# Kernel tuning notes

Hardware: AMD Instinct MI355X
Metric: run time of the kernel (lower is better)

The kernel has to match this reference:

```python
import jax, jax.numpy as jnp
import numpy as np

B, WIN, NN, F_IN, H = 8, 12, 2000, 8, 64
N = B * WIN * NN          # total graph nodes = 192000
E = 2_000_000             # edges
EPS = 1e-5                # BatchNorm eps
FC1_IN = 2 * H + WIN * F_IN + 1  # 225


def setup_inputs() -> dict:
    key = jax.random.key(0)
    ks = jax.random.split(key, 24)
    s = lambda k, shp: (jax.random.normal(k, shp, jnp.float32) * 0.05)
    d = {}
    d["adj_indices"] = jax.random.randint(ks[0], (2, E), 0, N)
    d["adj_weight"] = jax.random.uniform(ks[1], (E,), jnp.float32)
    d["x"] = jax.random.normal(ks[2], (N, F_IN), jnp.float32)
    d["inner_out"] = jax.random.normal(ks[3], (B * NN,), jnp.float32)
    # GCN layers
    d["W1"] = s(ks[4], (F_IN, H)); d["b1"] = jnp.zeros((H,), jnp.float32)
    d["W2"] = s(ks[5], (H, H));    d["b2"] = jnp.zeros((H,), jnp.float32)
    # BatchNorm affine params
    d["g1"] = jnp.ones((H,), jnp.float32);  d["be1"] = jnp.zeros((H,), jnp.float32)
    d["g2"] = jnp.ones((H,), jnp.float32);  d["be2"] = jnp.zeros((H,), jnp.float32)
    # LSTM 1 (input 2H) and LSTM 2 (input H); torch gate order i,f,g,o
    d["Wih1"] = s(ks[6], (4 * H, 2 * H)); d["Whh1"] = s(ks[7], (4 * H, H))
    d["bih1"] = jnp.zeros((4 * H,), jnp.float32); d["bhh1"] = jnp.zeros((4 * H,), jnp.float32)
    d["Wih2"] = s(ks[8], (4 * H, H)); d["Whh2"] = s(ks[9], (4 * H, H))
    d["bih2"] = jnp.zeros((4 * H,), jnp.float32); d["bhh2"] = jnp.zeros((4 * H,), jnp.float32)
    # FC head
    d["fc1_w"] = s(ks[10], (FC1_IN, H)); d["fc1_b"] = jnp.zeros((H,), jnp.float32)
    d["fc3_w"] = s(ks[11], (H, 1));      d["fc3_b"] = jnp.zeros((1,), jnp.float32)
    return d


def gcn(x, W, b, row, col, w):
    # PyG GCNConv: add self loops (weight 1), symmetric deg^-1/2 normalization,
    # aggregate messages from row (source) into col (target).
    loop = jnp.arange(N)
    r = jnp.concatenate([row, loop])
    c = jnp.concatenate([col, loop])
    ww = jnp.concatenate([w, jnp.ones((N,), w.dtype)])
    deg = jax.ops.segment_sum(ww, c, num_segments=N)
    dis = jnp.where(deg > 0, 1.0 / jnp.sqrt(deg), 0.0)
    norm = dis[r] * ww * dis[c]                      # [E+N]
    h = x @ W                                        # [N,H]
    out = jax.ops.segment_sum(h[r] * norm[:, None], c, num_segments=N)
    return out + b


def bn(x, g, b):  # training-mode BatchNorm1d (batch stats, biased var)
    m = x.mean(0)
    v = x.var(0)
    return (x - m) / jnp.sqrt(v + EPS) * g + b


def lstm(xs, Wih, Whh, bih, bhh):
    # xs: [T, Bn, D]; returns (all hidden states [T,Bn,H], last hidden [Bn,H])
    Bn = xs.shape[1]
    h0 = jnp.zeros((Bn, H), xs.dtype)
    def step(carry, xt):
        h, c = carry
        gates = xt @ Wih.T + h @ Whh.T + bih + bhh
        i, f, g, o = jnp.split(gates, 4, axis=-1)
        c = jax.nn.sigmoid(f) * c + jax.nn.sigmoid(i) * jnp.tanh(g)
        h = jax.nn.sigmoid(o) * jnp.tanh(c)
        return (h, c), h
    (hT, _), ys = jax.lax.scan(step, (h0, h0), xs)
    return ys, hT


def reference(adj_indices, adj_weight, x, inner_out,
              W1, b1, W2, b2, g1, be1, g2, be2,
              Wih1, Whh1, bih1, bhh1, Wih2, Whh2, bih2, bhh2,
              fc1_w, fc1_b, fc3_w, fc3_b):
    row, col = adj_indices[0], adj_indices[1]
    skip = x.reshape(B, WIN, NN, F_IN).transpose(0, 2, 1, 3).reshape(B * NN, WIN * F_IN)
    h1 = bn(jax.nn.relu(gcn(x, W1, b1, row, col, adj_weight)), g1, be1)   # dropout = identity (eval)
    h2 = bn(jax.nn.relu(gcn(h1, W2, b2, row, col, adj_weight)), g2, be2)
    h = jnp.concatenate([h1, h2], axis=1)                                  # [N, 2H]
    seq = h.reshape(B, WIN, NN, 2 * H).transpose(1, 0, 2, 3).reshape(WIN, B * NN, 2 * H)
    y1, hn1 = lstm(seq, Wih1, Whh1, bih1, bhh1)
    _, hn2 = lstm(y1, Wih2, Whh2, bih2, bhh2)
    z = jnp.concatenate([hn1, hn2, inner_out[:, None], skip], axis=1)      # [B*NN, FC1_IN]
    z = jax.nn.relu(z @ fc1_w + fc1_b)
    z = jax.nn.relu(z @ fc3_w + fc3_b)
    return z.reshape(-1)                                                   # [B*NN]
```

## Files before the change

### kernel.cpp

```cpp
#include <hip/hip_runtime.h>
#include <math.h>

#define N_NODES 192000
#define EDGES   2000000
#define HID     64
#define BN_ROWS 16000
#define T_WIN   12
#define B_SZ    8
#define NN_SZ   2000
#define FIN     8
#define BN_EPS  1e-5f

typedef _Float16 f16x2 __attribute__((ext_vector_type(2)));
typedef _Float16 half4 __attribute__((ext_vector_type(4)));
typedef _Float16 half8 __attribute__((ext_vector_type(8)));
typedef float    f32x4 __attribute__((ext_vector_type(4)));
union F16x2U { float f; f16x2 h; };

__device__ __forceinline__ float frcp(float x){
#if __has_builtin(__builtin_amdgcn_rcpf)
    return __builtin_amdgcn_rcpf(x);
#else
    return 1.0f/x;
#endif
}
__device__ __forceinline__ float fsig(float x){ return frcp(1.0f + __expf(-x)); }
__device__ __forceinline__ float ftanh(float x){ return fmaf(2.0f, fsig(2.0f*x), -1.0f); }

__device__ __forceinline__ float packf16(float a, float b){
    F16x2U u; u.h[0] = (_Float16)a; u.h[1] = (_Float16)b; return u.f;
}

__global__ void edge_pre(const int* __restrict__ col, const float* __restrict__ w,
                         unsigned long long* __restrict__ dc, int* __restrict__ rank){
    int e = blockIdx.x*blockDim.x + threadIdx.x;
    if (e < EDGES){
        int c = col[e];
        unsigned int fx = (unsigned int)(w[e]*16777216.0f + 0.5f);
        unsigned long long old = atomicAdd(&dc[c], (1ULL << 32) | (unsigned long long)fx);
        rank[e] = (int)(old >> 32);
    }
}

__global__ void scanA(const unsigned long long* __restrict__ dc,
                      int* __restrict__ excl, int* __restrict__ bsum){
    __shared__ int sm[256];
    int i = blockIdx.x*256 + threadIdx.x;
    int v = (int)(dc[i] >> 32);
    sm[threadIdx.x] = v;
    __syncthreads();
    #pragma unroll
    for (int off = 1; off < 256; off <<= 1){
        int t = (threadIdx.x >= off) ? sm[threadIdx.x - off] : 0;
        __syncthreads();
        sm[threadIdx.x] += t;
        __syncthreads();
    }
    excl[i] = sm[threadIdx.x] - v;
    if (threadIdx.x == 255) bsum[blockIdx.x] = sm[255];
}

__global__ void scanB(const int* __restrict__ bsum, int* __restrict__ bscan, int nb){
    __shared__ int sm[1024];
    int tid = threadIdx.x;
    int v = (tid < nb) ? bsum[tid] : 0;
    sm[tid] = v;
    __syncthreads();
    #pragma unroll
    for (int off = 1; off < 1024; off <<= 1){
        int t = (tid >= off) ? sm[tid - off] : 0;
        __syncthreads();
        sm[tid] += t;
        __syncthreads();
    }
    bscan[tid] = sm[tid] - v;
}

__global__ void scanC(const int* __restrict__ excl, const int* __restrict__ bscan,
                      const unsigned long long* __restrict__ dc,
                      float* __restrict__ dis, int* __restrict__ offsets){
    int i = blockIdx.x*256 + threadIdx.x;
    offsets[i] = excl[i] + bscan[i >> 8];
    float deg = (float)(unsigned int)(dc[i] & 0xffffffffULL) * (1.0f/16777216.0f);
    dis[i] = rsqrtf(deg + 1.0f);
    if (i == N_NODES-1) offsets[N_NODES] = EDGES;
}

__global__ void build_csr(const int* __restrict__ row, const int* __restrict__ col,
                          const float* __restrict__ w, const int* __restrict__ rank,
                          const float* __restrict__ dis, const int* __restrict__ offsets,
                          int2* __restrict__ edge_s){
    int e = blockIdx.x*blockDim.x + threadIdx.x;
    if (e >= EDGES) return;
    int r = row[e], c = col[e];
    float nr = dis[r]*w[e]*dis[c];
    int p = offsets[c] + rank[e];
    int2 ev; ev.x = r; ev.y = __float_as_int(nr);
    edge_s[p] = ev;
}

__global__ __launch_bounds__(256) void aggx_k(
        const int* __restrict__ offsets, const int2* __restrict__ edge_s,
        const float* __restrict__ dis, const float* __restrict__ x,
        float* __restrict__ ax){
    int g   = blockIdx.x*32 + (threadIdx.x >> 3);
    int sub = threadIdx.x & 7;
    float d = dis[g];
    float acc = x[(size_t)g*8 + sub]*d*d;
    int k  = offsets[g];
    int k1 = offsets[g+1];
    for (; k+4 <= k1; k += 4){
        int2 e0 = edge_s[k], e1 = edge_s[k+1], e2 = edge_s[k+2], e3 = edge_s[k+3];
        float v0 = x[(size_t)e0.x*8 + sub];
        float v1 = x[(size_t)e1.x*8 + sub];
        float v2 = x[(size_t)e2.x*8 + sub];
        float v3 = x[(size_t)e3.x*8 + sub];
        acc += v0*__int_as_float(e0.y);
        acc += v1*__int_as_float(e1.y);
        acc += v2*__int_as_float(e2.y);
        acc += v3*__int_as_float(e3.y);
    }
    for (; k < k1; k++){
        int2 e0 = edge_s[k];
        acc += x[(size_t)e0.x*8 + sub]*__int_as_float(e0.y);
    }
    ax[(size_t)g*8 + sub] = acc;
}

__global__ __launch_bounds__(256) void lin1b_stats(
        const float* __restrict__ ax, const float* __restrict__ W1,
        const float* __restrict__ b1, float* __restrict__ out,
        float* __restrict__ gsum, float* __restrict__ gsq){
    __shared__ float Ws[512];
    for (int i = threadIdx.x; i < 512; i += 256) Ws[i] = W1[i];
    __syncthreads();
    int f = threadIdx.x & 63;
    float wc[8];
    #pragma unroll
    for (int q = 0; q < 8; q++) wc[q] = Ws[q*64 + f];
    float bb = b1[f];
    float s = 0.f, s2 = 0.f;
    int stride = gridDim.x*blockDim.x;
    for (int idx = blockIdx.x*blockDim.x + threadIdx.x; idx < N_NODES*64; idx += stride){
        int j = idx >> 6;
        const float* ar = ax + (size_t)j*8;
        float acc = bb;
        #pragma unroll
        for (int q = 0; q < 8; q++) acc += ar[q]*wc[q];
        float v = fmaxf(acc, 0.f);
        out[idx] = v;
        s += v; s2 += v*v;
    }
    __shared__ float s1m[256], s2m[256];
    s1m[threadIdx.x] = s; s2m[threadIdx.x] = s2;
    __syncthreads();
    if (threadIdx.x < 64){
        float t1 = s1m[threadIdx.x]+s1m[threadIdx.x+64]+s1m[threadIdx.x+128]+s1m[threadIdx.x+192];
        float t2 = s2m[threadIdx.x]+s2m[threadIdx.x+64]+s2m[threadIdx.x+128]+s2m[threadIdx.x+192];
        atomicAdd(&gsum[threadIdx.x], t1);
        atomicAdd(&gsq[threadIdx.x], t2);
    }
}

#define L2ROWS 128
#define XS2    132
__global__ __launch_bounds__(128) void lin2_bn(
        const float* __restrict__ gcnA, const float* __restrict__ gsum,
        const float* __restrict__ gsq, const float* __restrict__ g1,
        const float* __restrict__ be1, const float* __restrict__ W2,
        _Float16* __restrict__ h1H, float* __restrict__ hlinH){
    __shared__ float Ws[64*64];
    __shared__ float xsT[64*XS2];
    int tid = threadIdx.x;
    int r0 = blockIdx.x * L2ROWS;

    for (int i = tid; i < 1024; i += 128)
        *(float4*)&Ws[i*4] = *(const float4*)&W2[i*4];

    int k4 = tid & 15;
    int rb = tid >> 4;
    float scv[4], shv[4];
    #pragma unroll
    for (int q = 0; q < 4; q++){
        int f = k4*4 + q;
        float mean = gsum[f]*(1.0f/(float)N_NODES);
        float var  = fmaxf(gsq[f]*(1.0f/(float)N_NODES) - mean*mean, 0.f);
        float sc_  = g1[f]*rsqrtf(var + BN_EPS);
        scv[q] = sc_; shv[q] = be1[f] - mean*sc_;
    }
    for (int it = 0; it < 16; it++){
        int r = it*8 + rb;
        float4 v = *(const float4*)&gcnA[(size_t)(r0+r)*64 + k4*4];
        v.x = v.x*scv[0]+shv[0]; v.y = v.y*scv[1]+shv[1];
        v.z = v.z*scv[2]+shv[2]; v.w = v.w*scv[3]+shv[3];
        half4 hh;
        hh[0]=(_Float16)v.x; hh[1]=(_Float16)v.y; hh[2]=(_Float16)v.z; hh[3]=(_Float16)v.w;
        *(half4*)&h1H[(size_t)(r0+r)*64 + k4*4] = hh;
        xsT[(k4*4+0)*XS2 + r] = v.x;
        xsT[(k4*4+1)*XS2 + r] = v.y;
        xsT[(k4*4+2)*XS2 + r] = v.z;
        xsT[(k4*4+3)*XS2 + r] = v.w;
    }
    __syncthreads();

    int cg = tid & 7;
    int rg = tid >> 3;
    float acc[8][8];
    #pragma unroll
    for (int i = 0; i < 8; i++)
        #pragma unroll
        for (int j = 0; j < 8; j++) acc[i][j] = 0.f;

    float4 a0 = *(float4*)&xsT[0*XS2 + rg*8];
    float4 a1 = *(float4*)&xsT[0*XS2 + rg*8 + 4];
    float4 w0 = *(float4*)&Ws[0*64 + cg*8];
    float4 w1 = *(float4*)&Ws[0*64 + cg*8 + 4];
    for (int k = 0; k < 64; k++){
        float4 na0, na1, nw0, nw1;
        if (k < 63){
            na0 = *(float4*)&xsT[(k+1)*XS2 + rg*8];
            na1 = *(float4*)&xsT[(k+1)*XS2 + rg*8 + 4];
            nw0 = *(float4*)&Ws[(k+1)*64 + cg*8];
            nw1 = *(float4*)&Ws[(k+1)*64 + cg*8 + 4];
        }
        float ar[8] = {a0.x,a0.y,a0.z,a0.w,a1.x,a1.y,a1.z,a1.w};
        float wcv[8] = {w0.x,w0.y,w0.z,w0.w,w1.x,w1.y,w1.z,w1.w};
        #pragma unroll
        for (int i = 0; i < 8; i++)
            #pragma unroll
            for (int j = 0; j < 8; j++) acc[i][j] += ar[i]*wcv[j];
        a0=na0; a1=na1; w0=nw0; w1=nw1;
    }
    #pragma unroll
    for (int i = 0; i < 8; i++){
        size_t r = (size_t)(r0 + rg*8 + i);
        float4 pk;
        pk.x = packf16(acc[i][0], acc[i][1]);
        pk.y = packf16(acc[i][2], acc[i][3]);
        pk.z = packf16(acc[i][4], acc[i][5]);
        pk.w = packf16(acc[i][6], acc[i][7]);
        *(float4*)&hlinH[r*32 + cg*4] = pk;
    }
}

__global__ __launch_bounds__(256) void gather2h(
        const int* __restrict__ offsets, const int2* __restrict__ edge_s,
        const float* __restrict__ dis, const float* __restrict__ hlinH,
        const float* __restrict__ bias, float* __restrict__ g2Hf){
    int j = blockIdx.x*8 + (threadIdx.x >> 5);
    int p = threadIdx.x & 31;
    float d = dis[j];
    float dd = d*d;
    F16x2U u; u.f = hlinH[(size_t)j*32 + p];
    float ax = (float)u.h[0]*dd;
    float ay = (float)u.h[1]*dd;
    int k  = offsets[j];
    int k1 = offsets[j+1];
    for (; k+4 <= k1; k += 4){
        int2 e0 = edge_s[k], e1 = edge_s[k+1], e2 = edge_s[k+2], e3 = edge_s[k+3];
        F16x2U a, b, c, e;
        a.f = hlinH[(size_t)e0.x*32 + p];
        b.f = hlinH[(size_t)e1.x*32 + p];
        c.f = hlinH[(size_t)e2.x*32 + p];
        e.f = hlinH[(size_t)e3.x*32 + p];
        float n0 = __int_as_float(e0.y), n1 = __int_as_float(e1.y);
        float n2 = __int_as_float(e2.y), n3 = __int_as_float(e3.y);
        ax += (float)a.h[0]*n0; ay += (float)a.h[1]*n0;
        ax += (float)b.h[0]*n1; ay += (float)b.h[1]*n1;
        ax += (float)c.h[0]*n2; ay += (float)c.h[1]*n2;
        ax += (float)e.h[0]*n3; ay += (float)e.h[1]*n3;
    }
    for (; k < k1; k++){
        int2 e0 = edge_s[k];
        F16x2U a; a.f = hlinH[(size_t)e0.x*32 + p];
        float n0 = __int_as_float(e0.y);
        ax += (float)a.h[0]*n0; ay += (float)a.h[1]*n0;
    }
    float2 bv = *(const float2*)&bias[2*p];
    float vx = fmaxf(ax + bv.x, 0.f);
    float vy = fmaxf(ay + bv.y, 0.f);
    F16x2U o; o.h[0] = (_Float16)vx; o.h[1] = (_Float16)vy;
    g2Hf[(size_t)j*32 + p] = o.f;
}

__global__ __launch_bounds__(256) void stats2h(
        const float* __restrict__ g2Hf, float* __restrict__ gsum2, float* __restrict__ gsq2){
    int p = threadIdx.x & 31;
    float s0 = 0.f, s1 = 0.f, q0 = 0.f, q1 = 0.f;
    int stride = gridDim.x*blockDim.x;
    for (int idx = blockIdx.x*blockDim.x + threadIdx.x; idx < N_NODES*32; idx += stride){
        F16x2U u; u.f = g2Hf[idx];
        float vx = (float)u.h[0], vy = (float)u.h[1];
        s0 += vx; q0 += vx*vx;
        s1 += vy; q1 += vy*vy;
    }
    __shared__ float sb[128];
    if (threadIdx.x < 128) sb[threadIdx.x] = 0.f;
    __syncthreads();
    atomicAdd(&sb[2*p],      s0);
    atomicAdd(&sb[2*p+1],    s1);
    atomicAdd(&sb[64+2*p],   q0);
    atomicAdd(&sb[64+2*p+1], q1);
    __syncthreads();
    if (threadIdx.x < 64){
        atomicAdd(&gsum2[threadIdx.x], sb[threadIdx.x]);
        atomicAdd(&gsq2[threadIdx.x],  sb[64+threadIdx.x]);
    }
}

__global__ void prep_weights(const float* __restrict__ Wih1, const float* __restrict__ Whh1,
                             const float* __restrict__ bih1, const float* __restrict__ bhh1,
                             const float* __restrict__ Wih2, const float* __restrict__ Whh2,
                             const float* __restrict__ bih2, const float* __restrict__ bhh2,
                             _Float16* W1F, _Float16* W2F, float* b1c, float* b2c){
    int idx = blockIdx.x*blockDim.x + threadIdx.x;
    if (idx < 6*256*32){
        int kt = idx >> 13;
        int rem = idx & 8191;
        int n = rem >> 5, kin = rem & 31;
        int k = kt*32 + kin;
        float v = (k < 128) ? Wih1[n*128 + k] : Whh1[n*64 + (k-128)];
        W1F[idx] = (_Float16)v;
    }
    int i2 = idx - 6*256*32;
    if (i2 >= 0 && i2 < 4*256*32){
        int kt = i2 >> 13;
        int rem = i2 & 8191;
        int n = rem >> 5, kin = rem & 31;
        int k = kt*32 + kin;
        float v = (k < 64) ? Wih2[n*64 + k] : Whh2[n*64 + (k-64)];
        W2F[i2] = (_Float16)v;
    }
    int i3 = idx - (6*256*32 + 4*256*32);
    if (i3 >= 0 && i3 < 256) b1c[i3] = bih1[i3] + bhh1[i3];
    int i4 = i3 - 256;
    if (i4 >= 0 && i4 < 256) b2c[i4] = bih2[i4] + bhh2[i4];
}

#define X1S 200
#define X2S 136
__global__ __launch_bounds__(256) void lstm_fused(
        const _Float16* __restrict__ h1H, const _Float16* __restrict__ g2H,
        const float* __restrict__ gsum2, const float* __restrict__ gsq2,
        const float* __restrict__ g2bn, const float* __restrict__ be2,
        const _Float16* __restrict__ W1F, const _Float16* __restrict__ W2F,
        const float* __restrict__ b1c, const float* __restrict__ b2c,
        float* __restrict__ h1s, float* __restrict__ h2s){
    __shared__ _Float16 X1h[16*X1S];
    __shared__ _Float16 X2h[16*X2S];
    int tid = threadIdx.x;
    int j0 = blockIdx.x*16;
    int w    = tid >> 6;
    int lane = tid & 63;
    int quad = lane >> 4;
    int l16  = lane & 15;
    int u    = 16*w + l16;

    int c4 = tid & 15;
    int sr = (tid >> 4) & 15;
    int sj = j0 + sr;
    int sb = sj / NN_SZ, sn = sj - sb*NN_SZ;
    size_t rbase = ((size_t)(sb*T_WIN)*NN_SZ + sn)*64 + c4*4;
    float sc2v[4], sh2v[4];
    #pragma unroll
    for (int q = 0; q < 4; q++){
        int f = c4*4 + q;
        float mean = gsum2[f]*(1.0f/(float)N_NODES);
        float var  = fmaxf(gsq2[f]*(1.0f/(float)N_NODES) - mean*mean, 0.f);
        float sc_  = g2bn[f]*rsqrtf(var + BN_EPS);
        sc2v[q] = sc_; sh2v[q] = be2[f] - mean*sc_;
    }

    float c1r[4], c2r[4], h2r[4];
    #pragma unroll
    for (int i = 0; i < 4; i++){ c1r[i] = 0.f; c2r[i] = 0.f; h2r[i] = 0.f; }

    float bi1 = b1c[u], bf1 = b1c[64+u], bg1 = b1c[128+u], bo1 = b1c[192+u];
    float bi2 = b2c[u], bf2 = b2c[64+u], bg2 = b2c[128+u], bo2 = b2c[192+u];

    {
        half4 v0 = *(const half4*)&h1H[rbase];
        half4 g4 = *(const half4*)&g2H[rbase];
        half4 v1;
        #pragma unroll
        for (int q = 0; q < 4; q++) v1[q] = (_Float16)((float)g4[q]*sc2v[q] + sh2v[q]);
        *(half4*)&X1h[sr*X1S + c4*4]       = v0;
        *(half4*)&X1h[sr*X1S + 64 + c4*4]  = v1;
        *(half4*)&X1h[sr*X1S + 128 + c4*4] = (half4){0,0,0,0};
    }
    __syncthreads();

    for (int t = 0; t < T_WIN; t++){
        half4 nv0, ng4;
        if (t < T_WIN-1){
            size_t rb = rbase + (size_t)(t+1)*NN_SZ*64;
            nv0 = *(const half4*)&h1H[rb];
            ng4 = *(const half4*)&g2H[rb];
        }

        f32x4 acc[4];
        #pragma unroll
        for (int g = 0; g < 4; g++) acc[g] = (f32x4){0.f,0.f,0.f,0.f};
        #pragma unroll
        for (int kt = 0; kt < 6; kt++){
            half8 a = *(const half8*)&X1h[l16*X1S + kt*32 + quad*8];
            #pragma unroll
            for (int g = 0; g < 4; g++){
                half8 b = *(const half8*)&W1F[(size_t)(kt*256 + 64*g + u)*32 + quad*8];
                acc[g] = __builtin_amdgcn_mfma_f32_16x16x32_f16(a, b, acc[g], 0, 0, 0);
            }
        }
        __syncthreads();

        #pragma unroll
        for (int r = 0; r < 4; r++){
            int rowl = quad*4 + r;
            float gi = acc[0][r] + bi1;
            float gf = acc[1][r] + bf1;
            float gg = acc[2][r] + bg1;
            float go = acc[3][r] + bo1;
            float cn = fsig(gf)*c1r[r] + fsig(gi)*ftanh(gg);
            float hn = fsig(go)*ftanh(cn);
            c1r[r] = cn;
            X2h[rowl*X2S + u]      = (_Float16)hn;
            X2h[rowl*X2S + 64 + u] = (_Float16)h2r[r];
            X1h[rowl*X1S + 128 + u] = (_Float16)hn;
            if (t == T_WIN-1) h1s[(size_t)(j0 + rowl)*64 + u] = hn;
        }
        if (t < T_WIN-1){
            half4 v1;
            #pragma unroll
            for (int q = 0; q < 4; q++) v1[q] = (_Float16)((float)ng4[q]*sc2v[q] + sh2v[q]);
            *(half4*)&X1h[sr*X1S + c4*4]      = nv0;
            *(half4*)&X1h[sr*X1S + 64 + c4*4] = v1;
        }
        __syncthreads();

        f32x4 acc2[4];
        #pragma unroll
        for (int g = 0; g < 4; g++) acc2[g] = (f32x4){0.f,0.f,0.f,0.f};
        #pragma unroll
        for (int kt = 0; kt < 4; kt++){
            half8 a = *(const half8*)&X2h[l16*X2S + kt*32 + quad*8];
            #pragma unroll
            for (int g = 0; g < 4; g++){
                half8 b = *(const half8*)&W2F[(size_t)(kt*256 + 64*g + u)*32 + quad*8];
                acc2[g] = __builtin_amdgcn_mfma_f32_16x16x32_f16(a, b, acc2[g], 0, 0, 0);
            }
        }

        #pragma unroll
        for (int r = 0; r < 4; r++){
            int rowl = quad*4 + r;
            float gi = acc2[0][r] + bi2;
            float gf = acc2[1][r] + bf2;
            float gg = acc2[2][r] + bg2;
            float go = acc2[3][r] + bo2;
            float cn = fsig(gf)*c2r[r] + fsig(gi)*ftanh(gg);
            float hn = fsig(go)*ftanh(cn);
            c2r[r] = cn;
            h2r[r] = hn;
            if (t == T_WIN-1) h2s[(size_t)(j0 + rowl)*64 + u] = hn;
        }
    }
}

__global__ __launch_bounds__(256) void fc_head(
        const float* __restrict__ h1s, const float* __restrict__ h2s,
        const float* __restrict__ inner, const float* __restrict__ x,
        const float* __restrict__ fc1_w, const float* __restrict__ fc1_b,
        const float* __restrict__ fc3_w, const float* __restrict__ fc3_b,
        float* __restrict__ out){
    __shared__ float zsm[4][226];
    int wv = threadIdx.x >> 6;
    int f  = threadIdx.x & 63;
    int j  = blockIdx.x*4 + wv;
    int b = j / NN_SZ, n = j - b*NN_SZ;
    for (int k = f; k < 225; k += 64){
        float v;
        if (k < 64)        v = h1s[j*64 + k];
        else if (k < 128)  v = h2s[j*64 + (k-64)];
        else if (k == 128) v = inner[j];
        else {
            int kk = k - 129;
            int w_ = kk >> 3, ff = kk & 7;
            v = x[((b*T_WIN + w_)*NN_SZ + n)*FIN + ff];
        }
        zsm[wv][k] = v;
    }
    __syncthreads();
    float acc = fc1_b[f];
    for (int k = 0; k < 225; k++) acc += zsm[wv][k]*fc1_w[k*64 + f];
    float p = fmaxf(acc, 0.f) * fc3_w[f];
    #pragma unroll
    for (int off = 32; off > 0; off >>= 1) p += __shfl_down(p, off, 64);
    if (f == 0) out[j] = fmaxf(p + fc3_b[0], 0.f);
}

extern "C" void kernel_launch(void* const* d_in, const int* in_sizes, int n_in,
                              void* d_out, int out_size, void* d_ws, size_t ws_size,
                              hipStream_t stream){
    const int*   adj  = (const int*)d_in[0];
    const int*   row  = adj;
    const int*   col  = adj + EDGES;
    const float* aw   = (const float*)d_in[1];
    const float* x    = (const float*)d_in[2];
    const float* inner= (const float*)d_in[3];
    const float* W1   = (const float*)d_in[4];
    const float* b1   = (const float*)d_in[5];
    const float* W2   = (const float*)d_in[6];
    const float* b2   = (const float*)d_in[7];
    const float* g1   = (const float*)d_in[8];
    const float* be1  = (const float*)d_in[9];
    const float* g2   = (const float*)d_in[10];
    const float* be2  = (const float*)d_in[11];
    const float* Wih1 = (const float*)d_in[12];
    const float* Whh1 = (const float*)d_in[13];
    const float* bih1 = (const float*)d_in[14];
    const float* bhh1 = (const float*)d_in[15];
    const float* Wih2 = (const float*)d_in[16];
    const float* Whh2 = (const float*)d_in[17];
    const float* bih2 = (const float*)d_in[18];
    const float* bhh2 = (const float*)d_in[19];
    const float* fc1w = (const float*)d_in[20];
    const float* fc1b = (const float*)d_in[21];
    const float* fc3w = (const float*)d_in[22];
    const float* fc3b = (const float*)d_in[23];
    float* out = (float*)d_out;

    float* ws = (float*)d_ws;
    const size_t NB = (size_t)N_NODES*64;
    float* bufX = ws;
    float* bufY = ws + NB;
    float* bufZ = ws + 2*NB;
    int2*  edge_s  = (int2*)(ws + 3*NB);
    float* degdis  = ws + 3*NB + (size_t)2*EDGES;
    float* gsum    = degdis + N_NODES;
    float* gsq     = gsum + 64;
    float* gsum2   = gsq + 64;
    float* gsq2    = gsum2 + 64;
    unsigned long long* dc = (unsigned long long*)(gsq2 + 64);
    int* excl    = (int*)(dc + N_NODES);
    int* bsum    = excl + N_NODES;
    int* bscan   = bsum + 1024;
    int* offsets = bscan + 1024;
    int* rank    = offsets + (N_NODES+2);

    float* hlinH = bufX;
    _Float16* h1H = (_Float16*)bufZ;
    float* ax    = bufZ + (size_t)N_NODES*32 + 64;
    float* gcnA1 = bufY;
    float* g2Hf  = bufY;

    float* h1s = bufX;
    float* h2s = bufX + (size_t)BN_ROWS*64;
    _Float16* W1F = (_Float16*)(bufX + (size_t)4*BN_ROWS*64);
    _Float16* W2F = W1F + 6*256*32;
    float* b1c = (float*)(W2F + 4*256*32);
    float* b2c = b1c + 256;

    hipMemsetAsync(dc, 0, N_NODES*sizeof(unsigned long long), stream);
    hipMemsetAsync(gsum, 0, 256*sizeof(float), stream);
    edge_pre <<<(EDGES+255)/256, 256, 0, stream>>>(col, aw, dc, rank);
    scanA    <<<750, 256, 0, stream>>>(dc, excl, bsum);
    scanB    <<<1, 1024, 0, stream>>>(bsum, bscan, 750);
    scanC    <<<750, 256, 0, stream>>>(excl, bscan, dc, degdis, offsets);
    build_csr<<<(EDGES+255)/256, 256, 0, stream>>>(row, col, aw, rank, degdis, offsets, edge_s);

    aggx_k<<<N_NODES/32, 256, 0, stream>>>(offsets, edge_s, degdis, x, ax);
    lin1b_stats<<<1024, 256, 0, stream>>>(ax, W1, b1, gcnA1, gsum, gsq);

    lin2_bn<<<N_NODES/L2ROWS, 128, 0, stream>>>(gcnA1, gsum, gsq, g1, be1, W2, h1H, hlinH);

    gather2h<<<N_NODES/8, 256, 0, stream>>>(offsets, edge_s, degdis, hlinH, b2, g2Hf);
    stats2h<<<1024, 256, 0, stream>>>(g2Hf, gsum2, gsq2);

    prep_weights<<<(6*256*32 + 4*256*32 + 512 + 255)/256, 256, 0, stream>>>(
        Wih1, Whh1, bih1, bhh1, Wih2, Whh2, bih2, bhh2, W1F, W2F, b1c, b2c);
    lstm_fused<<<BN_ROWS/16, 256, 0, stream>>>(h1H, (const _Float16*)g2Hf,
                                               gsum2, gsq2, g2, be2,
                                               W1F, W2F, b1c, b2c, h1s, h2s);

    fc_head<<<BN_ROWS/4, 256, 0, stream>>>(h1s, h2s, inner, x, fc1w, fc1b, fc3w, fc3b, out);
}
```

Before: 569.1 us.

## Build CSR via two-level bucket sort with shared-memory atomics

Replaces the global per-node 64-bit atomic histogram, three-pass scan and random scatter with a coarse 256-node bucket histogram in shared memory, a single-block bucket scan, a bucketed scatter, and a per-bucket CSR finalize that stages edges in LDS. Source-side normalization dis[row] is no longer folded into edge weights; the gather kernels now load dis[row] per edge instead. This is meant to cut global atomic contention and scattered writes in graph preprocessing. The cost is an extra random dis load per edge in both aggregation kernels, plus a slow fallback path when a bucket exceeds LDS capacity.

```diff
diff --git a/kernel.cpp b/kernel.cpp
--- a/kernel.cpp
+++ b/kernel.cpp
@@ -11,6 +11,11 @@
 #define FIN     8
 #define BN_EPS  1e-5f
 
+#define NBKT    750
+#define NBLKA   1024
+#define ACHUNK  1956
+#define BKT_CAP 5120
+
 typedef _Float16 f16x2 __attribute__((ext_vector_type(2)));
 typedef _Float16 half4 __attribute__((ext_vector_type(4)));
 typedef _Float16 half8 __attribute__((ext_vector_type(8)));
@@ -31,39 +36,33 @@
     F16x2U u; u.h[0] = (_Float16)a; u.h[1] = (_Float16)b; return u.f;
 }
 
-__global__ void edge_pre(const int* __restrict__ col, const float* __restrict__ w,
-                         unsigned long long* __restrict__ dc, int* __restrict__ rank){
-    int e = blockIdx.x*blockDim.x + threadIdx.x;
-    if (e < EDGES){
-        int c = col[e];
-        unsigned int fx = (unsigned int)(w[e]*16777216.0f + 0.5f);
-        unsigned long long old = atomicAdd(&dc[c], (1ULL << 32) | (unsigned long long)fx);
-        rank[e] = (int)(old >> 32);
-    }
-}
-
-__global__ void scanA(const unsigned long long* __restrict__ dc,
-                      int* __restrict__ excl, int* __restrict__ bsum){
-    __shared__ int sm[256];
-    int i = blockIdx.x*256 + threadIdx.x;
-    int v = (int)(dc[i] >> 32);
-    sm[threadIdx.x] = v;
-    __syncthreads();
-    #pragma unroll
-    for (int off = 1; off < 256; off <<= 1){
-        int t = (threadIdx.x >= off) ? sm[threadIdx.x - off] : 0;
-        __syncthreads();
-        sm[threadIdx.x] += t;
-        __syncthreads();
-    }
-    excl[i] = sm[threadIdx.x] - v;
-    if (threadIdx.x == 255) bsum[blockIdx.x] = sm[255];
-}
-
-__global__ void scanB(const int* __restrict__ bsum, int* __restrict__ bscan, int nb){
+__global__ __launch_bounds__(256) void hist_coarse(
+        const int* __restrict__ col, unsigned* __restrict__ gcount,
+        int* __restrict__ blockbase){
+    __shared__ unsigned bh[NBKT];
+    int bl = blockIdx.x, tid = threadIdx.x;
+    for (int i = tid; i < NBKT; i += 256) bh[i] = 0u;
+    __syncthreads();
+    int e0 = bl*ACHUNK;
+    int e1 = e0 + ACHUNK; if (e1 > EDGES) e1 = EDGES;
+    for (int e = e0 + tid*4; e < e1; e += 1024){
+        int4 c4 = *(const int4*)&col[e];
+        atomicAdd(&bh[((unsigned)c4.x) >> 8], 1u);
+        atomicAdd(&bh[((unsigned)c4.y) >> 8], 1u);
+        atomicAdd(&bh[((unsigned)c4.z) >> 8], 1u);
+        atomicAdd(&bh[((unsigned)c4.w) >> 8], 1u);
+    }
+    __syncthreads();
+    for (int i = tid; i < NBKT; i += 256)
+        blockbase[bl*NBKT + i] = (int)atomicAdd(&gcount[i], bh[i]);
+}
+
+__global__ __launch_bounds__(1024) void scan_bkt(
+        const unsigned* __restrict__ gcount, int* __restrict__ gbase,
+        int* __restrict__ offsets){
     __shared__ int sm[1024];
     int tid = threadIdx.x;
-    int v = (tid < nb) ? bsum[tid] : 0;
+    int v = (tid < NBKT) ? (int)gcount[tid] : 0;
     sm[tid] = v;
     __syncthreads();
     #pragma unroll
@@ -73,30 +72,90 @@
         sm[tid] += t;
         __syncthreads();
     }
-    bscan[tid] = sm[tid] - v;
-}
-
-__global__ void scanC(const int* __restrict__ excl, const int* __restrict__ bscan,
-                      const unsigned long long* __restrict__ dc,
-                      float* __restrict__ dis, int* __restrict__ offsets){
-    int i = blockIdx.x*256 + threadIdx.x;
-    offsets[i] = excl[i] + bscan[i >> 8];
-    float deg = (float)(unsigned int)(dc[i] & 0xffffffffULL) * (1.0f/16777216.0f);
-    dis[i] = rsqrtf(deg + 1.0f);
-    if (i == N_NODES-1) offsets[N_NODES] = EDGES;
-}
-
-__global__ void build_csr(const int* __restrict__ row, const int* __restrict__ col,
-                          const float* __restrict__ w, const int* __restrict__ rank,
-                          const float* __restrict__ dis, const int* __restrict__ offsets,
-                          int2* __restrict__ edge_s){
-    int e = blockIdx.x*blockDim.x + threadIdx.x;
-    if (e >= EDGES) return;
-    int r = row[e], c = col[e];
-    float nr = dis[r]*w[e]*dis[c];
-    int p = offsets[c] + rank[e];
-    int2 ev; ev.x = r; ev.y = __float_as_int(nr);
-    edge_s[p] = ev;
+    if (tid < NBKT) gbase[tid] = sm[tid] - v;
+    if (tid == NBKT) gbase[NBKT] = EDGES;
+    if (tid == NBKT+1) offsets[N_NODES] = EDGES;
+}
+
+__global__ __launch_bounds__(256) void scatter_bucket(
+        const int* __restrict__ row, const int* __restrict__ col,
+        const float* __restrict__ w, const int* __restrict__ blockbase,
+        const int* __restrict__ gbase, int2* __restrict__ rec){
+    __shared__ unsigned cur[NBKT];
+    int bl = blockIdx.x, tid = threadIdx.x;
+    for (int i = tid; i < NBKT; i += 256)
+        cur[i] = (unsigned)(gbase[i] + blockbase[bl*NBKT + i]);
+    __syncthreads();
+    int e0 = bl*ACHUNK;
+    int e1 = e0 + ACHUNK; if (e1 > EDGES) e1 = EDGES;
+    for (int e = e0 + tid*4; e < e1; e += 1024){
+        int4 r4 = *(const int4*)&row[e];
+        int4 c4 = *(const int4*)&col[e];
+        float4 w4 = *(const float4*)&w[e];
+        int cc[4] = {c4.x, c4.y, c4.z, c4.w};
+        int rr[4] = {r4.x, r4.y, r4.z, r4.w};
+        float wf[4] = {w4.x, w4.y, w4.z, w4.w};
+        #pragma unroll
+        for (int q = 0; q < 4; q++){
+            int c = cc[q];
+            unsigned wfix = (unsigned)(wf[q]*16777216.0f + 0.5f);
+            if (wfix > 0xFFFFFFu) wfix = 0xFFFFFFu;
+            unsigned p = atomicAdd(&cur[((unsigned)c) >> 8], 1u);
+            int2 rv; rv.x = rr[q];
+            rv.y = (int)((((unsigned)(c & 255)) << 24) | wfix);
+            rec[p] = rv;
+        }
+    }
+}
+
+__global__ __launch_bounds__(256) void bucket_csr(
+        const int2* __restrict__ rec, const int* __restrict__ gbase,
+        int2* __restrict__ edge_s, int* __restrict__ offsets,
+        float* __restrict__ dis){
+    __shared__ int2 S[BKT_CAP];
+    __shared__ unsigned cnt[256];
+    __shared__ unsigned wsum[256];
+    __shared__ unsigned cur[256];
+    __shared__ float dloc[256];
+    int b = blockIdx.x, tid = threadIdx.x;
+    int k0 = gbase[b], k1 = gbase[b+1];
+    int n = k1 - k0;
+    cnt[tid] = 0u; wsum[tid] = 0u;
+    __syncthreads();
+    bool staged = (n <= BKT_CAP);
+    for (int i = tid; i < n; i += 256){
+        int2 r = rec[k0 + i];
+        if (staged) S[i] = r;
+        unsigned clow = ((unsigned)r.y) >> 24;
+        atomicAdd(&cnt[clow], 1u);
+        atomicAdd(&wsum[clow], ((unsigned)r.y) & 0xFFFFFFu);
+    }
+    __syncthreads();
+    unsigned v = cnt[tid];
+    float deg = (float)wsum[tid] * (1.0f/16777216.0f);
+    float dv = rsqrtf(deg + 1.0f);
+    dloc[tid] = dv;
+    dis[(b<<8) + tid] = dv;
+    #pragma unroll
+    for (int off = 1; off < 256; off <<= 1){
+        unsigned t = (tid >= off) ? cnt[tid - off] : 0u;
+        __syncthreads();
+        cnt[tid] += t;
+        __syncthreads();
+    }
+    unsigned excl = cnt[tid] - v;
+    cur[tid] = excl;
+    offsets[(b<<8) + tid] = k0 + (int)excl;
+    __syncthreads();
+    for (int i = tid; i < n; i += 256){
+        int2 r = staged ? S[i] : rec[k0 + i];
+        unsigned clow = ((unsigned)r.y) >> 24;
+        unsigned wfix = ((unsigned)r.y) & 0xFFFFFFu;
+        float sv = (float)wfix * (1.0f/16777216.0f) * dloc[clow];
+        unsigned p = atomicAdd(&cur[clow], 1u);
+        int2 o; o.x = r.x; o.y = __float_as_int(sv);
+        edge_s[k0 + (int)p] = o;
+    }
 }
 
 __global__ __launch_bounds__(256) void aggx_k(
@@ -111,18 +170,19 @@
     int k1 = offsets[g+1];
     for (; k+4 <= k1; k += 4){
         int2 e0 = edge_s[k], e1 = edge_s[k+1], e2 = edge_s[k+2], e3 = edge_s[k+3];
+        float d0 = dis[e0.x], d1 = dis[e1.x], d2 = dis[e2.x], d3 = dis[e3.x];
         float v0 = x[(size_t)e0.x*8 + sub];
         float v1 = x[(size_t)e1.x*8 + sub];
         float v2 = x[(size_t)e2.x*8 + sub];
         float v3 = x[(size_t)e3.x*8 + sub];
-        acc += v0*__int_as_float(e0.y);
-        acc += v1*__int_as_float(e1.y);
-        acc += v2*__int_as_float(e2.y);
-        acc += v3*__int_as_float(e3.y);
+        acc += v0*(d0*__int_as_float(e0.y));
+        acc += v1*(d1*__int_as_float(e1.y));
+        acc += v2*(d2*__int_as_float(e2.y));
+        acc += v3*(d3*__int_as_float(e3.y));
     }
     for (; k < k1; k++){
         int2 e0 = edge_s[k];
-        acc += x[(size_t)e0.x*8 + sub]*__int_as_float(e0.y);
+        acc += x[(size_t)e0.x*8 + sub]*(dis[e0.x]*__int_as_float(e0.y));
     }
     ax[(size_t)g*8 + sub] = acc;
 }
@@ -258,13 +318,14 @@
     int k1 = offsets[j+1];
     for (; k+4 <= k1; k += 4){
         int2 e0 = edge_s[k], e1 = edge_s[k+1], e2 = edge_s[k+2], e3 = edge_s[k+3];
+        float d0 = dis[e0.x], d1 = dis[e1.x], d2 = dis[e2.x], d3 = dis[e3.x];
         F16x2U a, b, c, e;
         a.f = hlinH[(size_t)e0.x*32 + p];
         b.f = hlinH[(size_t)e1.x*32 + p];
         c.f = hlinH[(size_t)e2.x*32 + p];
         e.f = hlinH[(size_t)e3.x*32 + p];
-        float n0 = __int_as_float(e0.y), n1 = __int_as_float(e1.y);
-        float n2 = __int_as_float(e2.y), n3 = __int_as_float(e3.y);
+        float n0 = d0*__int_as_float(e0.y), n1 = d1*__int_as_float(e1.y);
+        float n2 = d2*__int_as_float(e2.y), n3 = d3*__int_as_float(e3.y);
         ax += (float)a.h[0]*n0; ay += (float)a.h[1]*n0;
         ax += (float)b.h[0]*n1; ay += (float)b.h[1]*n1;
         ax += (float)c.h[0]*n2; ay += (float)c.h[1]*n2;
@@ -273,7 +334,7 @@
     for (; k < k1; k++){
         int2 e0 = edge_s[k];
         F16x2U a; a.f = hlinH[(size_t)e0.x*32 + p];
-        float n0 = __int_as_float(e0.y);
+        float n0 = dis[e0.x]*__int_as_float(e0.y);
         ax += (float)a.h[0]*n0; ay += (float)a.h[1]*n0;
     }
     float2 bv = *(const float2*)&bias[2*p];
@@ -539,12 +600,12 @@
     float* gsq     = gsum + 64;
     float* gsum2   = gsq + 64;
     float* gsq2    = gsum2 + 64;
-    unsigned long long* dc = (unsigned long long*)(gsq2 + 64);
-    int* excl    = (int*)(dc + N_NODES);
-    int* bsum    = excl + N_NODES;
-    int* bscan   = bsum + 1024;
-    int* offsets = bscan + 1024;
-    int* rank    = offsets + (N_NODES+2);
+    unsigned* gcount = (unsigned*)(gsq2 + 64);
+    int* gbase   = (int*)(gcount + NBKT);
+    int* offsets = gbase + (NBKT + 2);
+
+    int* blockbase = (int*)bufX;
+    int2* rec      = (int2*)bufY;
 
     float* hlinH = bufX;
     _Float16* h1H = (_Float16*)bufZ;
@@ -559,13 +620,12 @@
     float* b1c = (float*)(W2F + 4*256*32);
     float* b2c = b1c + 256;
 
-    hipMemsetAsync(dc, 0, N_NODES*sizeof(unsigned long long), stream);
+    hipMemsetAsync(gcount, 0, NBKT*sizeof(unsigned), stream);
     hipMemsetAsync(gsum, 0, 256*sizeof(float), stream);
-    edge_pre <<<(EDGES+255)/256, 256, 0, stream>>>(col, aw, dc, rank);
-    scanA    <<<750, 256, 0, stream>>>(dc, excl, bsum);
-    scanB    <<<1, 1024, 0, stream>>>(bsum, bscan, 750);
-    scanC    <<<750, 256, 0, stream>>>(excl, bscan, dc, degdis, offsets);
-    build_csr<<<(EDGES+255)/256, 256, 0, stream>>>(row, col, aw, rank, degdis, offsets, edge_s);
+    hist_coarse   <<<NBLKA, 256, 0, stream>>>(col, gcount, blockbase);
+    scan_bkt      <<<1, 1024, 0, stream>>>(gcount, gbase, offsets);
+    scatter_bucket<<<NBLKA, 256, 0, stream>>>(row, col, aw, blockbase, gbase, rec);
+    bucket_csr    <<<NBKT, 256, 0, stream>>>(rec, gbase, edge_s, offsets, degdis);
 
     aggx_k<<<N_NODES/32, 256, 0, stream>>>(offsets, edge_s, degdis, x, ax);
     lin1b_stats<<<1024, 256, 0, stream>>>(ax, W1, b1, gcnA1, gsum, gsq);
```

After: 514.7 us. -9.6%, faster.
